# Kernel tuning notes

Measured on AMD Instinct MI355X. Metric: run time of the kernel, lower is better.

## Reference

```python
import jax, jax.numpy as jnp
import numpy as np

B, T, D, H = 4, 1024, 1024, 16
HD = D // H
DFF = 2048          # ExpertTier hidden width
K = 3               # ConvTier causal kernel size
NEG = -1e9


def layernorm(x, w, b, eps=1e-5):
    m = jnp.mean(x, axis=-1, keepdims=True)
    v = jnp.var(x, axis=-1, keepdims=True)
    return (x - m) * jax.lax.rsqrt(v + eps) * w + b


def rope_cos_sin(t, hd):
    inv = 1.0 / (10000.0 ** (jnp.arange(0, hd, 2, dtype=jnp.float32) / hd))
    freqs = jnp.outer(jnp.arange(t, dtype=jnp.float32), inv)  # (T, hd/2)
    return jnp.cos(freqs), jnp.sin(freqs)


def apply_rope(x, cos, sin):
    # x: (B, H, T, hd); cos/sin: (T, hd/2)
    x1, x2 = jnp.split(x, 2, axis=-1)
    return jnp.concatenate([x1 * cos - x2 * sin, x1 * sin + x2 * cos], axis=-1)


def causal_attn(q, k, v):
    # q,k,v: (..., T, d); full causal softmax attention
    t = q.shape[-2]
    scale = 1.0 / jnp.sqrt(jnp.asarray(q.shape[-1], q.dtype))
    scores = jnp.einsum('...qd,...kd->...qk', q, k) * scale
    mask = jnp.triu(jnp.ones((t, t), dtype=bool), k=1)
    scores = jnp.where(mask, NEG, scores)
    w = jax.nn.softmax(scores, axis=-1)
    return jnp.einsum('...qk,...kd->...qd', w, v)


def setup_inputs() -> dict:
    key = jax.random.key(0)
    ks = jax.random.split(key, 16)
    ws = 0.02
    g = lambda k, shape, s: jax.random.normal(k, shape, dtype=jnp.float32) * s
    return {
        'x': g(ks[0], (B, T, D), 1.0),
        'ln1_w': jnp.ones((D,), jnp.float32), 'ln1_b': jnp.zeros((D,), jnp.float32),
        'qkv_w': g(ks[1], (D, 3 * D), ws),
        'out_w': g(ks[2], (D, D), ws),
        'ln2_w': jnp.ones((D,), jnp.float32), 'ln2_b': jnp.zeros((D,), jnp.float32),
        'router_w': g(ks[3], (D, 4), ws),
        'conv_w': g(ks[4], (D, 1, K), 0.1),             # depthwise OIW, groups=D
        'expert_w1': g(ks[5], (D, DFF), ws),
        'expert_w2': g(ks[6], (DFF, D), ws),
        'at_wq': g(ks[7], (D, D), ws),
        'at_wk': g(ks[8], (D, D), ws),
        'at_wv': g(ks[9], (D, D), ws),
        'at_wo': g(ks[10], (D, D), ws),
        'tier_gate': jnp.full((D,), 0.1, jnp.float32),
        'sink_kv_scale': jnp.asarray(0.1, jnp.float32),
    }


def reference(x, ln1_w, ln1_b, qkv_w, out_w, ln2_w, ln2_b, router_w, conv_w,
              expert_w1, expert_w2, at_wq, at_wk, at_wv, at_wo,
              tier_gate, sink_kv_scale):
    b, t, d = x.shape
    # --- backbone causal self-attention with RoPE (pre-norm) ---
    h1 = layernorm(x, ln1_w, ln1_b)
    qkv = (h1 @ qkv_w).reshape(b, t, 3, H, HD)
    q = qkv[:, :, 0].transpose(0, 2, 1, 3)  # (B,H,T,hd)
    k = qkv[:, :, 1].transpose(0, 2, 1, 3)
    v = qkv[:, :, 2].transpose(0, 2, 1, 3)
    cos, sin = rope_cos_sin(t, HD)
    q = apply_rope(q, cos, sin)
    k = apply_rope(k, cos, sin)
    ao = causal_attn(q, k, v)                         # (B,H,T,hd)
    ao = ao.transpose(0, 2, 1, 3).reshape(b, t, d) @ out_w
    x = x + ao
    # --- router + tiers ---
    h = layernorm(x, ln2_w, ln2_b)
    routing_w = jax.nn.softmax(h @ router_w, axis=-1)  # (B,T,4): conv/expert/attn/sink
    # ConvTier: depthwise causal conv (k=3) + GELU
    hc = jnp.pad(h.transpose(0, 2, 1), ((0, 0), (0, 0), (K - 1, 0)))  # (B,D,T+K-1)
    conv = jax.lax.conv_general_dilated(hc, conv_w, (1,), 'VALID',
                                        feature_group_count=d,
                                        dimension_numbers=('NCH', 'OIH', 'NCH'))
    conv_out = jax.nn.gelu(conv.transpose(0, 2, 1))   # (B,T,D)
    # ExpertTier: 2-layer GELU MLP
    expert_out = jax.nn.gelu(h @ expert_w1) @ expert_w2
    # AttentionTier: single-head causal attention
    attn2 = causal_attn(h @ at_wq, h @ at_wk, h @ at_wv) @ at_wo
    # SinkTier outputs zeros -> contributes nothing to the weighted sum
    combined = (conv_out * routing_w[..., 0:1]
                + expert_out * routing_w[..., 1:2]
                + attn2 * routing_w[..., 2:3])
    x = x + combined * tier_gate
    # sink kv scaling
    kv_scale = 1.0 - routing_w[..., 3] * (1.0 - jnp.abs(sink_kv_scale))
    x = x * kv_scale[..., None]
    return (x, routing_w)
```

## Files before the change

kernel.cpp:

```cpp
#include <hip/hip_runtime.h>

#define Bz 4
#define Tz 1024
#define Dz 1024
#define Hz 16
#define NTz (Bz*Tz)

typedef short s8v __attribute__((ext_vector_type(8)));
typedef float f4v __attribute__((ext_vector_type(4)));

__device__ __forceinline__ float bf2f(unsigned short u){
  unsigned int x = ((unsigned int)u) << 16;
  return __builtin_bit_cast(float, x);
}
__device__ __forceinline__ unsigned short f2bf(float f){
  unsigned int x = __builtin_bit_cast(unsigned int, f);
  x += 0x7fffu + ((x >> 16) & 1u);
  return (unsigned short)(x >> 16);
}
__device__ __forceinline__ float gelu_f(float x){
  float z = 1.5957691216057308f * (x + 0.044715f * x * x * x);
  return x / (1.0f + __expf(-z));
}
__device__ __forceinline__ void gl16(const unsigned short* g, unsigned short* l){
  __builtin_amdgcn_global_load_lds(
      (const __attribute__((address_space(1))) unsigned int*)g,
      (__attribute__((address_space(3))) unsigned int*)l, 16, 0, 0);
}

struct WSeg { const float* in; unsigned short* out; int R, C, blk0, bx; };
struct WPack { WSeg s[8]; };
__global__ __launch_bounds__(256) void k_convtrans_all(WPack p)
{
  __shared__ float tile[32][33];
  int bid = blockIdx.x;
  const float* in = p.s[0].in; unsigned short* out = p.s[0].out;
  int R = p.s[0].R, C = p.s[0].C, blk0 = 0, bx = p.s[0].bx;
  #pragma unroll
  for (int i = 1; i < 8; ++i) {
    if (bid >= p.s[i].blk0) {
      in = p.s[i].in; out = p.s[i].out; R = p.s[i].R; C = p.s[i].C;
      blk0 = p.s[i].blk0; bx = p.s[i].bx;
    }
  }
  int rel = bid - blk0;
  int c0 = (rel % bx) * 32, r0 = (rel / bx) * 32;
  int tx = threadIdx.x & 31, ty = threadIdx.x >> 5;
  #pragma unroll
  for (int i = 0; i < 32; i += 8)
    tile[ty + i][tx] = in[(long)(r0 + ty + i) * C + c0 + tx];
  __syncthreads();
  #pragma unroll
  for (int i = 0; i < 32; i += 8)
    out[(long)(c0 + ty + i) * R + r0 + tx] = f2bf(tile[tx][ty + i]);
}

__global__ __launch_bounds__(256) void k_layernorm(const float* __restrict__ x,
    const float* __restrict__ w, const float* __restrict__ b,
    unsigned short* __restrict__ out)
{
  int row = blockIdx.x, tid = threadIdx.x;
  const float4* xp = (const float4*)(x + (long)row * Dz);
  float4 v = xp[tid];
  float s  = v.x + v.y + v.z + v.w;
  float ss = v.x*v.x + v.y*v.y + v.z*v.z + v.w*v.w;
  int lane = tid & 63, wv = tid >> 6;
  #pragma unroll
  for (int off = 32; off; off >>= 1){ s += __shfl_xor(s, off); ss += __shfl_xor(ss, off); }
  __shared__ float red[8];
  if (lane == 0){ red[wv] = s; red[4 + wv] = ss; }
  __syncthreads();
  s  = red[0] + red[1] + red[2] + red[3];
  ss = red[4] + red[5] + red[6] + red[7];
  float mean = s * (1.0f / Dz);
  float var  = ss * (1.0f / Dz) - mean * mean;
  float rstd = rsqrtf(var + 1e-5f);
  float4 wg = ((const float4*)w)[tid];
  float4 bg = ((const float4*)b)[tid];
  ushort4 ov;
  ov.x = f2bf((v.x - mean) * rstd * wg.x + bg.x);
  ov.y = f2bf((v.y - mean) * rstd * wg.y + bg.y);
  ov.z = f2bf((v.z - mean) * rstd * wg.z + bg.z);
  ov.w = f2bf((v.w - mean) * rstd * wg.w + bg.w);
  *((ushort4*)(out + (long)row * Dz) + tid) = ov;
}

__global__ __launch_bounds__(256) void k_ln_router(const unsigned short* __restrict__ x2,
    const float* __restrict__ w, const float* __restrict__ b,
    const float* __restrict__ rw, unsigned short* __restrict__ out,
    float* __restrict__ rout)
{
  int row = blockIdx.x, tid = threadIdx.x;
  ushort4 xu = *((const ushort4*)(x2 + (long)row * Dz) + tid);
  float4 v = {bf2f(xu.x), bf2f(xu.y), bf2f(xu.z), bf2f(xu.w)};
  float s  = v.x + v.y + v.z + v.w;
  float ss = v.x*v.x + v.y*v.y + v.z*v.z + v.w*v.w;
  int lane = tid & 63, wv = tid >> 6;
  #pragma unroll
  for (int off = 32; off; off >>= 1){ s += __shfl_xor(s, off); ss += __shfl_xor(ss, off); }
  __shared__ float red[8];
  if (lane == 0){ red[wv] = s; red[4 + wv] = ss; }
  __syncthreads();
  s  = red[0] + red[1] + red[2] + red[3];
  ss = red[4] + red[5] + red[6] + red[7];
  float mean = s * (1.0f / Dz);
  float var  = ss * (1.0f / Dz) - mean * mean;
  float rstd = rsqrtf(var + 1e-5f);
  float4 wg = ((const float4*)w)[tid];
  float4 bg = ((const float4*)b)[tid];
  float h0 = (v.x - mean) * rstd * wg.x + bg.x;
  float h1 = (v.y - mean) * rstd * wg.y + bg.y;
  float h2 = (v.z - mean) * rstd * wg.z + bg.z;
  float h3 = (v.w - mean) * rstd * wg.w + bg.w;
  ushort4 ov;
  ov.x = f2bf(h0); ov.y = f2bf(h1); ov.z = f2bf(h2); ov.w = f2bf(h3);
  *((ushort4*)(out + (long)row * Dz) + tid) = ov;
  int d0 = tid * 4;
  float4 r0 = *(const float4*)(rw + (long)d0 * 4);
  float4 r1 = *(const float4*)(rw + (long)(d0 + 1) * 4);
  float4 r2 = *(const float4*)(rw + (long)(d0 + 2) * 4);
  float4 r3 = *(const float4*)(rw + (long)(d0 + 3) * 4);
  float a0 = h0*r0.x + h1*r1.x + h2*r2.x + h3*r3.x;
  float a1 = h0*r0.y + h1*r1.y + h2*r2.y + h3*r3.y;
  float a2 = h0*r0.z + h1*r1.z + h2*r2.z + h3*r3.z;
  float a3 = h0*r0.w + h1*r1.w + h2*r2.w + h3*r3.w;
  #pragma unroll
  for (int off = 32; off; off >>= 1) {
    a0 += __shfl_xor(a0, off); a1 += __shfl_xor(a1, off);
    a2 += __shfl_xor(a2, off); a3 += __shfl_xor(a3, off);
  }
  __shared__ float red2[4][4];
  if (lane == 0){ red2[wv][0] = a0; red2[wv][1] = a1; red2[wv][2] = a2; red2[wv][3] = a3; }
  __syncthreads();
  if (tid == 0) {
    float s0 = red2[0][0] + red2[1][0] + red2[2][0] + red2[3][0];
    float s1 = red2[0][1] + red2[1][1] + red2[2][1] + red2[3][1];
    float s2 = red2[0][2] + red2[1][2] + red2[2][2] + red2[3][2];
    float s3 = red2[0][3] + red2[1][3] + red2[2][3] + red2[3][3];
    float mx = fmaxf(fmaxf(s0, s1), fmaxf(s2, s3));
    float e0 = __expf(s0 - mx), e1 = __expf(s1 - mx);
    float e2 = __expf(s2 - mx), e3 = __expf(s3 - mx);
    float inv = 1.0f / (e0 + e1 + e2 + e3);
    float4 r = {e0 * inv, e1 * inv, e2 * inv, e3 * inv};
    *(float4*)(rout + (long)row * 4) = r;
  }
}

__global__ __launch_bounds__(512) void k_gemm512(
    const unsigned short* __restrict__ A,
    const unsigned short* __restrict__ Bt,
    unsigned short* __restrict__ Cb)
{
  constexpr int BK = 64;
  __shared__ unsigned short As[2][128 * BK];
  __shared__ unsigned short Bs[2][128 * BK];
  int lin = blockIdx.y * gridDim.x + blockIdx.x;
  int cols = gridDim.x, rows = gridDim.y;
  int nwg = cols * rows;
  if ((nwg & 7) == 0) lin = (lin & 7) * (nwg >> 3) + (lin >> 3);
  int in_grp = 8 * cols;
  int gid = lin / in_grp;
  int fm = gid * 8;
  int gsz = min(rows - fm, 8);
  int rem = lin - gid * in_grp;
  int pm = fm + (rem % gsz);
  int pn = rem / gsz;
  int bm = pm * 128, bn = pn * 128;

  int tid = threadIdx.x, w = tid >> 6, lane = tid & 63;
  int fr = lane & 15, fg = lane >> 4;
  int sw = (fr & 7) * 8;
  int wr = (w >> 1) * 32, wc = (w & 1) * 64;
  int lrow = lane >> 3;
  int lcol = ((lane & 7) ^ lrow) * 8;

  const unsigned short* AgJ[2];
  const unsigned short* BgJ[2];
  int OffJ[2];
  #pragma unroll
  for (int j = 0; j < 2; ++j) {
    AgJ[j] = A  + (long)(bm + j * 64 + w * 8 + lrow) * 1024 + lcol;
    BgJ[j] = Bt + (long)(bn + j * 64 + w * 8 + lrow) * 1024 + lcol;
    OffJ[j] = (j * 64 + w * 8) * BK;
  }

  f4v acc[2][4];
  #pragma unroll
  for (int m = 0; m < 2; ++m)
    #pragma unroll
    for (int n = 0; n < 4; ++n)
      acc[m][n] = (f4v){0.f, 0.f, 0.f, 0.f};

  auto stage = [&](int buf, int k0){
    #pragma unroll
    for (int j = 0; j < 2; ++j) gl16(AgJ[j] + k0, &As[buf][OffJ[j]]);
    #pragma unroll
    for (int j = 0; j < 2; ++j) gl16(BgJ[j] + k0, &Bs[buf][OffJ[j]]);
  };
  auto compute = [&](int buf){
    #pragma unroll
    for (int kk = 0; kk < 2; ++kk) {
      int kg = (kk * 32 + fg * 8) ^ sw;
      s8v af[2], bfv[4];
      #pragma unroll
      for (int m = 0; m < 2; ++m) af[m]  = *(const s8v*)&As[buf][(wr + m * 16 + fr) * BK + kg];
      #pragma unroll
      for (int n = 0; n < 4; ++n) bfv[n] = *(const s8v*)&Bs[buf][(wc + n * 16 + fr) * BK + kg];
      #pragma unroll
      for (int m = 0; m < 2; ++m)
        #pragma unroll
        for (int n = 0; n < 4; ++n)
          acc[m][n] = __builtin_amdgcn_mfma_f32_16x16x32_bf16(af[m], bfv[n], acc[m][n], 0, 0, 0);
    }
  };

  int cur = 0;
  stage(0, 0);
  __syncthreads();
  for (int k0 = 0; k0 < 1024; k0 += BK) {
    if (k0 + BK < 1024) stage(cur ^ 1, k0 + BK);
    compute(cur);
    __syncthreads();
    cur ^= 1;
  }

  int cr = bm + wr + fg * 4, cc = bn + wc + fr;
  #pragma unroll
  for (int m = 0; m < 2; ++m)
    #pragma unroll
    for (int n = 0; n < 4; ++n)
      #pragma unroll
      for (int i = 0; i < 4; ++i) {
        long row = cr + m * 16 + i;
        long col = cc + n * 16;
        float v = acc[m][n][i];
        if (col < 2048) v = gelu_f(v);
        Cb[row * 5120 + col] = f2bf(v);
      }
}

__global__ __launch_bounds__(512) void k_tail512(
    const unsigned short* __restrict__ tierb,
    const unsigned short* __restrict__ w_ew2t,
    unsigned short* __restrict__ eo, long eoDelta,
    unsigned short* __restrict__ Sb,
    unsigned short* __restrict__ v2t)
{
  constexpr int BK = 64;
  __shared__ unsigned short As[2][128 * BK];
  __shared__ unsigned short Bs[2][128 * BK];
  int bid = blockIdx.x;
  int tid = threadIdx.x;

  if (bid >= 656) {
    int g0 = (bid - 656) * 16;
    int sub = tid & 255, half = tid >> 8;
    int tx = sub & 31, ty = sub >> 5;
    unsigned short* T = &As[0][0] + half * 1100;
    for (int it = 0; it < 8; ++it) {
      int g = g0 + half * 8 + it;
      int z = g >> 10, rem = g & 1023;
      int r0 = (rem >> 5) * 32, c0 = (rem & 31) * 32;
      const unsigned short* inp = tierb + 4096 + (long)z * ((long)Tz * 5120);
      unsigned short* outp = v2t + (long)z * ((long)Tz * 1024);
      #pragma unroll
      for (int i = 0; i < 32; i += 8)
        T[(ty + i) * 33 + tx] = inp[(long)(r0 + ty + i) * 5120 + c0 + tx];
      __syncthreads();
      #pragma unroll
      for (int i = 0; i < 32; i += 8)
        outp[(long)(c0 + ty + i) * 1024 + r0 + tx] = T[tx * 33 + (ty + i)];
      __syncthreads();
    }
    return;
  }

  int w = tid >> 6, lane = tid & 63;
  int fr = lane & 15, fg = lane >> 4;
  int sw = (fr & 7) * 8;
  int wr = (w >> 1) * 32, wc = (w & 1) * 64;
  int lrow = lane >> 3;
  int lcol = ((lane & 7) ^ lrow) * 8;

  const unsigned short* A;
  const unsigned short* Bt;
  unsigned short* Cout;
  long ldA, ldB;
  int bm, bn;
  float scale;
  if (bid < 512) {
    int z = bid >> 8;
    int lin = bid & 255;
    lin = (lin & 7) * 32 + (lin >> 3);
    int gid = lin / 64;
    int fm = gid * 8;
    int rem = lin - gid * 64;
    int pm = fm + (rem & 7);
    int pn = rem >> 3;
    bm = pm * 128; bn = pn * 128;
    A    = tierb + (long)z * 1024;
    Bt   = w_ew2t + (long)z * 1024;
    Cout = eo + (long)z * eoDelta;
    ldA = 5120; ldB = 2048;
    scale = 1.0f;
  } else {
    int r2 = bid - 512;
    int li = r2 % 36;
    int z  = r2 / 36;
    int r = (int)((sqrtf(8.f * li + 1.f) - 1.f) * 0.5f);
    if ((r + 1) * (r + 2) / 2 <= li) ++r;
    if (r * (r + 1) / 2 > li) --r;
    bm = r * 128; bn = (li - r * (r + 1) / 2) * 128;
    A    = tierb + 2048 + (long)z * ((long)Tz * 5120);
    Bt   = tierb + 3072 + (long)z * ((long)Tz * 5120);
    Cout = Sb + (long)z * ((long)Tz * Tz);
    ldA = 5120; ldB = 5120;
    scale = 0.03125f;
  }

  const unsigned short* AgJ[2];
  const unsigned short* BgJ[2];
  int OffJ[2];
  #pragma unroll
  for (int j = 0; j < 2; ++j) {
    AgJ[j] = A  + (long)(bm + j * 64 + w * 8 + lrow) * ldA + lcol;
    BgJ[j] = Bt + (long)(bn + j * 64 + w * 8 + lrow) * ldB + lcol;
    OffJ[j] = (j * 64 + w * 8) * BK;
  }

  f4v acc[2][4];
  #pragma unroll
  for (int m = 0; m < 2; ++m)
    #pragma unroll
    for (int n = 0; n < 4; ++n)
      acc[m][n] = (f4v){0.f, 0.f, 0.f, 0.f};

  auto stage = [&](int buf, int k0){
    #pragma unroll
    for (int j = 0; j < 2; ++j) gl16(AgJ[j] + k0, &As[buf][OffJ[j]]);
    #pragma unroll
    for (int j = 0; j < 2; ++j) gl16(BgJ[j] + k0, &Bs[buf][OffJ[j]]);
  };
  auto compute = [&](int buf){
    #pragma unroll
    for (int kk = 0; kk < 2; ++kk) {
      int kg = (kk * 32 + fg * 8) ^ sw;
      s8v af[2], bfv[4];
      #pragma unroll
      for (int m = 0; m < 2; ++m) af[m]  = *(const s8v*)&As[buf][(wr + m * 16 + fr) * BK + kg];
      #pragma unroll
      for (int n = 0; n < 4; ++n) bfv[n] = *(const s8v*)&Bs[buf][(wc + n * 16 + fr) * BK + kg];
      #pragma unroll
      for (int m = 0; m < 2; ++m)
        #pragma unroll
        for (int n = 0; n < 4; ++n)
          acc[m][n] = __builtin_amdgcn_mfma_f32_16x16x32_bf16(af[m], bfv[n], acc[m][n], 0, 0, 0);
    }
  };

  int cur = 0;
  stage(0, 0);
  __syncthreads();
  for (int k0 = 0; k0 < 1024; k0 += BK) {
    if (k0 + BK < 1024) stage(cur ^ 1, k0 + BK);
    compute(cur);
    __syncthreads();
    cur ^= 1;
  }

  int cr = bm + wr + fg * 4, cc = bn + wc + fr;
  #pragma unroll
  for (int m = 0; m < 2; ++m)
    #pragma unroll
    for (int n = 0; n < 4; ++n)
      #pragma unroll
      for (int i = 0; i < 4; ++i) {
        long row = cr + m * 16 + i;
        long col = cc + n * 16;
        Cout[row * 1024 + col] = f2bf(acc[m][n][i] * scale);
      }
}

__global__ __launch_bounds__(512) void k_wo512(
    const unsigned short* __restrict__ A,
    const unsigned short* __restrict__ Bt,
    unsigned short* __restrict__ Cb, long sC)
{
  constexpr int BK = 64;
  __shared__ unsigned short As[2][128 * BK];
  __shared__ unsigned short Bs[2][128 * BK];
  A  += (long)blockIdx.z * 512;
  Bt += (long)blockIdx.z * 512;
  Cb += (long)blockIdx.z * sC;
  int lin = blockIdx.y * gridDim.x + blockIdx.x;
  int cols = gridDim.x, rows = gridDim.y;
  int nwg = cols * rows;
  if ((nwg & 7) == 0) lin = (lin & 7) * (nwg >> 3) + (lin >> 3);
  int in_grp = 8 * cols;
  int gid = lin / in_grp;
  int fm = gid * 8;
  int gsz = min(rows - fm, 8);
  int rem = lin - gid * in_grp;
  int pm = fm + (rem % gsz);
  int pn = rem / gsz;
  int bm = pm * 128, bn = pn * 128;

  int tid = threadIdx.x, w = tid >> 6, lane = tid & 63;
  int fr = lane & 15, fg = lane >> 4;
  int sw = (fr & 7) * 8;
  int wr = (w >> 1) * 32, wc = (w & 1) * 64;
  int lrow = lane >> 3;
  int lcol = ((lane & 7) ^ lrow) * 8;

  const unsigned short* AgJ[2];
  const unsigned short* BgJ[2];
  int OffJ[2];
  #pragma unroll
  for (int j = 0; j < 2; ++j) {
    AgJ[j] = A  + (long)(bm + j * 64 + w * 8 + lrow) * 1024 + lcol;
    BgJ[j] = Bt + (long)(bn + j * 64 + w * 8 + lrow) * 1024 + lcol;
    OffJ[j] = (j * 64 + w * 8) * BK;
  }

  f4v acc[2][4];
  #pragma unroll
  for (int m = 0; m < 2; ++m)
    #pragma unroll
    for (int n = 0; n < 4; ++n)
      acc[m][n] = (f4v){0.f, 0.f, 0.f, 0.f};

  auto stage = [&](int buf, int k0){
    #pragma unroll
    for (int j = 0; j < 2; ++j) gl16(AgJ[j] + k0, &As[buf][OffJ[j]]);
    #pragma unroll
    for (int j = 0; j < 2; ++j) gl16(BgJ[j] + k0, &Bs[buf][OffJ[j]]);
  };
  auto compute = [&](int buf){
    #pragma unroll
    for (int kk = 0; kk < 2; ++kk) {
      int kg = (kk * 32 + fg * 8) ^ sw;
      s8v af[2], bfv[4];
      #pragma unroll
      for (int m = 0; m < 2; ++m) af[m]  = *(const s8v*)&As[buf][(wr + m * 16 + fr) * BK + kg];
      #pragma unroll
      for (int n = 0; n < 4; ++n) bfv[n] = *(const s8v*)&Bs[buf][(wc + n * 16 + fr) * BK + kg];
      #pragma unroll
      for (int m = 0; m < 2; ++m)
        #pragma unroll
        for (int n = 0; n < 4; ++n)
          acc[m][n] = __builtin_amdgcn_mfma_f32_16x16x32_bf16(af[m], bfv[n], acc[m][n], 0, 0, 0);
    }
  };

  int cur = 0;
  stage(0, 0);
  __syncthreads();
  for (int k0 = 0; k0 < 512; k0 += BK) {
    if (k0 + BK < 512) stage(cur ^ 1, k0 + BK);
    compute(cur);
    __syncthreads();
    cur ^= 1;
  }

  int cr = bm + wr + fg * 4, cc = bn + wc + fr;
  #pragma unroll
  for (int m = 0; m < 2; ++m)
    #pragma unroll
    for (int n = 0; n < 4; ++n)
      #pragma unroll
      for (int i = 0; i < 4; ++i) {
        long row = cr + m * 16 + i;
        long col = cc + n * 16;
        Cb[row * 1024 + col] = f2bf(acc[m][n][i]);
      }
}

template<int MODE, int BN, bool TRIMAP, bool TRIK, bool DBUF>
__global__ __launch_bounds__(256) void k_gemm(
    const unsigned short* __restrict__ A,
    const unsigned short* __restrict__ Bt,
    float* __restrict__ Cf, unsigned short* __restrict__ Cb,
    const float* __restrict__ addsrc,
    unsigned short* __restrict__ P1, unsigned short* __restrict__ P2,
    int N, int K, int lda, int ldb,
    long sA, long sB, long sC)
{
  constexpr int BM = 128;
  constexpr int MREP = (BN == 128) ? 4 : 2;
  constexpr int NB = DBUF ? 2 : 1;
  __shared__ unsigned short As[NB][BM * 64];
  __shared__ unsigned short Bs[NB][BN * 64];
  int bm, bn;
  if (TRIMAP) {
    int li = blockIdx.x;
    int nwg = gridDim.x;
    if ((nwg & 7) == 0) li = (li & 7) * (nwg >> 3) + (li >> 3);
    int r = (int)((sqrtf(4.f * li + 1.f) - 1.f) * 0.5f);
    if ((r + 1) * (r + 2) <= li) ++r;
    if (r * (r + 1) > li) --r;
    bm = r * 128; bn = (li - r * (r + 1)) * BN;
  } else {
    int lin = blockIdx.y * gridDim.x + blockIdx.x;
    int nwg = gridDim.x * gridDim.y;
    if ((nwg & 7) == 0) lin = (lin & 7) * (nwg >> 3) + (lin >> 3);
    int cols = gridDim.x, rows = gridDim.y;
    constexpr int GM = 8;
    int in_grp = GM * cols;
    int gid = lin / in_grp;
    int fm = gid * GM;
    int gsz = min(rows - fm, GM);
    int rem = lin - gid * in_grp;
    int pm = fm + (rem % gsz);
    int pn = rem / gsz;
    if (TRIK) pm = rows - 1 - pm;
    bm = pm * BM; bn = pn * BN;
  }
  A  += (long)blockIdx.z * sA;
  Bt += (long)blockIdx.z * sB;
  int tid = threadIdx.x, w = tid >> 6, lane = tid & 63;
  int wr, wc;
  if (BN == 128) { wr = (w >> 1) * 64; wc = (w & 1) * 64; }
  else           { wr = w * 32;        wc = 0; }
  f4v acc[MREP][4];
  #pragma unroll
  for (int m = 0; m < MREP; ++m)
    #pragma unroll
    for (int n = 0; n < 4; ++n)
      acc[m][n] = (f4v){0.f, 0.f, 0.f, 0.f};

  int Keff = K;
  if (TRIK) Keff = min(K, bm + BM);

  int lrow = lane >> 3;
  int lcol = (((lane & 7) ^ lrow) * 8);
  const unsigned short* AgJ[4];
  int AsOff[4];
  #pragma unroll
  for (int j = 0; j < 4; ++j) {
    AgJ[j] = A + (long)(bm + w * 32 + j * 8 + lrow) * lda + lcol;
    AsOff[j] = (w * 32 + j * 8) * 64;
  }
  constexpr int BCH = BN / 8 / 4;
  const unsigned short* BgJ[BCH];
  int BsOff[BCH];
  #pragma unroll
  for (int j = 0; j < BCH; ++j) {
    BgJ[j] = Bt + (long)(bn + w * (BCH * 8) + j * 8 + lrow) * ldb + lcol;
    BsOff[j] = (w * (BCH * 8) + j * 8) * 64;
  }

  int fr = lane & 15, fg = lane >> 4;
  int sw = (fr & 7) * 8;

  auto stage = [&](int buf, int k0){
    #pragma unroll
    for (int j = 0; j < 4; ++j) gl16(AgJ[j] + k0, &As[buf][AsOff[j]]);
    #pragma unroll
    for (int j = 0; j < BCH; ++j) gl16(BgJ[j] + k0, &Bs[buf][BsOff[j]]);
  };
  auto compute = [&](int buf){
    #pragma unroll
    for (int kk = 0; kk < 2; ++kk) {
      int kg = (kk * 32 + fg * 8) ^ sw;
      s8v af[MREP], bfv[4];
      #pragma unroll
      for (int m = 0; m < MREP; ++m) af[m]  = *(const s8v*)&As[buf][(wr + m * 16 + fr) * 64 + kg];
      #pragma unroll
      for (int n = 0; n < 4; ++n)    bfv[n] = *(const s8v*)&Bs[buf][(wc + n * 16 + fr) * 64 + kg];
      #pragma unroll
      for (int m = 0; m < MREP; ++m)
        #pragma unroll
        for (int n = 0; n < 4; ++n)
          acc[m][n] = __builtin_amdgcn_mfma_f32_16x16x32_bf16(af[m], bfv[n], acc[m][n], 0, 0, 0);
    }
  };

  if (DBUF) {
    int cur = 0;
    stage(0, 0);
    __syncthreads();
    for (int k0 = 0; k0 < Keff; k0 += 64) {
      if (k0 + 64 < Keff) stage(cur ^ 1, k0 + 64);
      compute(cur);
      __syncthreads();
      cur ^= 1;
    }
  } else {
    for (int k0 = 0; k0 < Keff; k0 += 64) {
      __syncthreads();
      stage(0, k0);
      __syncthreads();
      compute(0);
    }
  }

  int cr0 = bm + wr + fg * 4;
  int cc0 = bn + wc + fr;

  if (MODE == 4) {
    int sect = bn >> 10;
    if (sect == 2) {
      #pragma unroll
      for (int m = 0; m < MREP; ++m)
        #pragma unroll
        for (int n = 0; n < 4; ++n)
          #pragma unroll
          for (int i = 0; i < 4; ++i) {
            int row = cr0 + m * 16 + i;
            int vcol = (bn - 2048) + wc + n * 16 + fr;
            P2[(long)row * 1024 + vcol] = f2bf(acc[m][n][i]);
          }
    } else {
      unsigned short* dst = (sect == 0) ? Cb : P1;
      float scl = (sect == 0) ? 0.125f : 1.0f;
      int head = ((bn & 1023) + wc) >> 6;
      float inv0 = exp2f(-(float)fr * 0.4152410118609203f);
      float inv1 = exp2f(-(float)(fr + 16) * 0.4152410118609203f);
      #pragma unroll
      for (int m = 0; m < MREP; ++m)
        #pragma unroll
        for (int i = 0; i < 4; ++i) {
          int row = cr0 + m * 16 + i;
          int t = row & 1023, bq = row >> 10;
          float a0 = (float)t * inv0, a1 = (float)t * inv1;
          float cs0 = __cosf(a0), sn0 = __sinf(a0);
          float cs1 = __cosf(a1), sn1 = __sinf(a1);
          float v0 = acc[m][0][i], v1 = acc[m][1][i];
          float v2 = acc[m][2][i], v3 = acc[m][3][i];
          long base = ((long)(bq * 16 + head)) * 65536 + (long)t * 64 + fr;
          dst[base]      = f2bf((v0 * cs0 - v2 * sn0) * scl);
          dst[base + 32] = f2bf((v0 * sn0 + v2 * cs0) * scl);
          dst[base + 16] = f2bf((v1 * cs1 - v3 * sn1) * scl);
          dst[base + 48] = f2bf((v1 * sn1 + v3 * cs1) * scl);
        }
    }
    return;
  }

  #pragma unroll
  for (int m = 0; m < MREP; ++m)
    #pragma unroll
    for (int n = 0; n < 4; ++n)
      #pragma unroll
      for (int i = 0; i < 4; ++i) {
        long row = cr0 + m * 16 + i, col = cc0 + n * 16;
        long idx = (long)blockIdx.z * sC + row * (long)N + col;
        float v = acc[m][n][i];
        if (MODE == 1 || MODE == 7) v += addsrc[idx];
        if (MODE == 6) v *= 0.03125f;
        if (MODE <= 1) Cf[idx] = v; else Cb[idx] = f2bf(v);
      }
}

__global__ __launch_bounds__(256) void k_attn_mfma(
    const unsigned short* __restrict__ Qb, const unsigned short* __restrict__ Kb,
    const unsigned short* __restrict__ Vt, unsigned short* __restrict__ ao)
{
  __shared__ unsigned short Ks[64][72];
  __shared__ unsigned short Vs[64][72];
  __shared__ unsigned short Ps[4][16][72];
  int qb = 15 - (blockIdx.x >> 6);
  int bh = blockIdx.x & 63;
  int b = bh >> 4, h = bh & 15;
  int t0 = qb * 64;
  int tid = threadIdx.x, w = tid >> 6, lane = tid & 63;
  int fr = lane & 15, fg = lane >> 4;

  const unsigned short* qp = Qb + (long)bh * Tz * 64 + (long)(t0 + w * 16 + fr) * 64 + fg * 8;
  s8v qf[2] = { *(const s8v*)qp, *(const s8v*)(qp + 32) };

  f4v o_acc[4];
  #pragma unroll
  for (int n = 0; n < 4; ++n) o_acc[n] = (f4v){0.f, 0.f, 0.f, 0.f};
  float m_[4] = {-1e30f, -1e30f, -1e30f, -1e30f};
  float l_[4] = {0.f, 0.f, 0.f, 0.f};

  int sr = tid >> 3, sc = (tid & 7) * 8;
  const unsigned short* Kg = Kb + (long)bh * Tz * 64 + (long)sr * 64 + sc;
  const unsigned short* Vg = Vt + (long)bh * 64 * Tz + (long)sr * Tz + sc;

  uint4 pk0, pk1, pv0, pv1;
  auto loadregs = [&](int k0){
    pk0 = *(const uint4*)(Kg + (long)k0 * 64);
    pk1 = *(const uint4*)(Kg + (long)(k0 + 32) * 64);
    pv0 = *(const uint4*)(Vg + k0);
    pv1 = *(const uint4*)(Vg + (long)32 * Tz + k0);
  };
  auto storelds = [&](){
    *(uint4*)&Ks[sr][sc]      = pk0;
    *(uint4*)&Ks[sr + 32][sc] = pk1;
    *(uint4*)&Vs[sr][sc]      = pv0;
    *(uint4*)&Vs[sr + 32][sc] = pv1;
  };

  loadregs(0);
  storelds();
  __syncthreads();

  for (int kt = 0; kt <= qb; ++kt) {
    int k0 = kt * 64;
    if (kt < qb) loadregs(k0 + 64);

    f4v sacc[4];
    #pragma unroll
    for (int n = 0; n < 4; ++n) sacc[n] = (f4v){0.f, 0.f, 0.f, 0.f};
    #pragma unroll
    for (int kk = 0; kk < 2; ++kk) {
      int kg = kk * 32 + fg * 8;
      #pragma unroll
      for (int n = 0; n < 4; ++n) {
        s8v bf = *(const s8v*)&Ks[n * 16 + fr][kg];
        sacc[n] = __builtin_amdgcn_mfma_f32_16x16x32_bf16(qf[kk], bf, sacc[n], 0, 0, 0);
      }
    }

    bool full = (kt < qb);
    float p[4][4], alpha[4];
    #pragma unroll
    for (int i = 0; i < 4; ++i) {
      int trow = t0 + w * 16 + fg * 4 + i;
      float mx = -1e30f;
      #pragma unroll
      for (int n = 0; n < 4; ++n) {
        float sval = sacc[n][i];
        if (!full) {
          int key = k0 + n * 16 + fr;
          sval = (key <= trow) ? sval : -1e30f;
        }
        p[n][i] = sval;
        mx = fmaxf(mx, sval);
      }
      mx = fmaxf(mx, __shfl_xor(mx, 1));
      mx = fmaxf(mx, __shfl_xor(mx, 2));
      mx = fmaxf(mx, __shfl_xor(mx, 4));
      mx = fmaxf(mx, __shfl_xor(mx, 8));
      float mnew = fmaxf(m_[i], mx);
      alpha[i] = __expf(m_[i] - mnew);
      m_[i] = mnew;
      float ps = 0.f;
      #pragma unroll
      for (int n = 0; n < 4; ++n) {
        float pv = __expf(p[n][i] - mnew);
        p[n][i] = pv;
        ps += pv;
      }
      ps += __shfl_xor(ps, 1); ps += __shfl_xor(ps, 2);
      ps += __shfl_xor(ps, 4); ps += __shfl_xor(ps, 8);
      l_[i] = l_[i] * alpha[i] + ps;
    }
    #pragma unroll
    for (int n = 0; n < 4; ++n)
      #pragma unroll
      for (int i = 0; i < 4; ++i)
        o_acc[n][i] *= alpha[i];
    #pragma unroll
    for (int n = 0; n < 4; ++n)
      #pragma unroll
      for (int i = 0; i < 4; ++i)
        Ps[w][fg * 4 + i][n * 16 + fr] = f2bf(p[n][i]);

    #pragma unroll
    for (int kk = 0; kk < 2; ++kk) {
      int kg = kk * 32 + fg * 8;
      s8v pa = *(const s8v*)&Ps[w][fr][kg];
      #pragma unroll
      for (int n = 0; n < 4; ++n) {
        s8v vb = *(const s8v*)&Vs[n * 16 + fr][kg];
        o_acc[n] = __builtin_amdgcn_mfma_f32_16x16x32_bf16(pa, vb, o_acc[n], 0, 0, 0);
      }
    }

    if (kt < qb) {
      __syncthreads();
      storelds();
      __syncthreads();
    }
  }

  float inv[4];
  #pragma unroll
  for (int i = 0; i < 4; ++i) inv[i] = 1.0f / l_[i];
  #pragma unroll
  for (int n = 0; n < 4; ++n)
    #pragma unroll
    for (int i = 0; i < 4; ++i) {
      int t = t0 + w * 16 + fg * 4 + i;
      ao[((long)(b * Tz + t)) * Dz + h * 64 + n * 16 + fr] = f2bf(o_acc[n][i] * inv[i]);
    }
}

__global__ __launch_bounds__(256) void k_softmax_causal(const unsigned short* __restrict__ S,
    unsigned short* __restrict__ P)
{
  long row = blockIdx.x;
  int t = (int)(row & (Tz - 1));
  int tid = threadIdx.x;
  const unsigned short* sp = S + row * Tz;
  ushort4 v = ((const ushort4*)sp)[tid];
  float vv[4];
  vv[0] = (tid*4 + 0 <= t) ? bf2f(v.x) : -1e30f;
  vv[1] = (tid*4 + 1 <= t) ? bf2f(v.y) : -1e30f;
  vv[2] = (tid*4 + 2 <= t) ? bf2f(v.z) : -1e30f;
  vv[3] = (tid*4 + 3 <= t) ? bf2f(v.w) : -1e30f;
  float mx = fmaxf(fmaxf(vv[0], vv[1]), fmaxf(vv[2], vv[3]));
  int lane = tid & 63, wv = tid >> 6;
  #pragma unroll
  for (int off = 32; off; off >>= 1) mx = fmaxf(mx, __shfl_xor(mx, off));
  __shared__ float red[8];
  if (lane == 0) red[wv] = mx;
  __syncthreads();
  mx = fmaxf(fmaxf(red[0], red[1]), fmaxf(red[2], red[3]));
  float p[4];
  float s = 0.f;
  #pragma unroll
  for (int i = 0; i < 4; ++i){ p[i] = __expf(vv[i] - mx); s += p[i]; }
  #pragma unroll
  for (int off = 32; off; off >>= 1) s += __shfl_xor(s, off);
  if (lane == 0) red[4 + wv] = s;
  __syncthreads();
  s = red[4] + red[5] + red[6] + red[7];
  float inv = 1.0f / s;
  ushort4 ov;
  ov.x = f2bf(p[0] * inv); ov.y = f2bf(p[1] * inv);
  ov.z = f2bf(p[2] * inv); ov.w = f2bf(p[3] * inv);
  *((ushort4*)(P + row * Tz) + tid) = ov;
}

__global__ __launch_bounds__(256) void k_combine(
    const unsigned short* __restrict__ x2, const unsigned short* __restrict__ hbf,
    const unsigned short* __restrict__ eoa, const unsigned short* __restrict__ eob,
    const unsigned short* __restrict__ ap, const unsigned short* __restrict__ ap2,
    const float* __restrict__ rout, const float* __restrict__ convw,
    const float* __restrict__ tg, const float* __restrict__ sinkp,
    float* __restrict__ outx)
{
  int row = blockIdx.x, tid = threadIdx.x;
  int t = row & (Tz - 1), b = row >> 10;
  int d0 = tid * 4;
  ushort4 xu = *(const ushort4*)(x2 + (long)row * Dz + d0);
  ushort4 ea = *(const ushort4*)(eoa + (long)row * Dz + d0);
  ushort4 eb = *(const ushort4*)(eob + (long)row * Dz + d0);
  ushort4 a4 = *(const ushort4*)(ap + (long)row * Dz + d0);
  ushort4 a42 = *(const ushort4*)(ap2 + (long)row * Dz + d0);
  float4 t4 = *(const float4*)(tg + d0);
  float4 r4 = *(const float4*)(rout + (long)row * 4);
  float sks = fabsf(sinkp[0]);
  float kv = 1.0f - r4.w * (1.0f - sks);
  const float4* cwp = (const float4*)(convw + (long)d0 * 3);
  float4 c0 = cwp[0], c1 = cwp[1], c2 = cwp[2];
  float cwf[12] = {c0.x, c0.y, c0.z, c0.w, c1.x, c1.y, c1.z, c1.w, c2.x, c2.y, c2.z, c2.w};
  float hv[3][4];
  #pragma unroll
  for (int tap = 0; tap < 3; ++tap) {
    int tt = t - 2 + tap;
    if (tt >= 0) {
      ushort4 hu = *((const ushort4*)(hbf + ((long)(b * Tz + tt)) * Dz + d0));
      hv[tap][0] = bf2f(hu.x); hv[tap][1] = bf2f(hu.y);
      hv[tap][2] = bf2f(hu.z); hv[tap][3] = bf2f(hu.w);
    } else {
      hv[tap][0] = 0.f; hv[tap][1] = 0.f; hv[tap][2] = 0.f; hv[tap][3] = 0.f;
    }
  }
  float ov[4];
  float xi[4] = {bf2f(xu.x), bf2f(xu.y), bf2f(xu.z), bf2f(xu.w)};
  float ei[4] = {bf2f(ea.x) + bf2f(eb.x), bf2f(ea.y) + bf2f(eb.y),
                 bf2f(ea.z) + bf2f(eb.z), bf2f(ea.w) + bf2f(eb.w)};
  float ai[4] = {bf2f(a4.x) + bf2f(a42.x), bf2f(a4.y) + bf2f(a42.y),
                 bf2f(a4.z) + bf2f(a42.z), bf2f(a4.w) + bf2f(a42.w)};
  float ti[4] = {t4.x, t4.y, t4.z, t4.w};
  #pragma unroll
  for (int i = 0; i < 4; ++i) {
    float conv = hv[0][i] * cwf[i*3 + 0] + hv[1][i] * cwf[i*3 + 1] + hv[2][i] * cwf[i*3 + 2];
    float comb = gelu_f(conv) * r4.x + ei[i] * r4.y + ai[i] * r4.z;
    ov[i] = (xi[i] + comb * ti[i]) * kv;
  }
  float4 res = {ov[0], ov[1], ov[2], ov[3]};
  *(float4*)(outx + (long)row * Dz + d0) = res;
}

extern "C" void kernel_launch(void* const* d_in, const int* in_sizes, int n_in,
                              void* d_out, int out_size, void* d_ws, size_t ws_size,
                              hipStream_t stream) {
  (void)in_sizes; (void)n_in; (void)out_size; (void)ws_size;
  const float* x       = (const float*)d_in[0];
  const float* ln1_w   = (const float*)d_in[1];
  const float* ln1_b   = (const float*)d_in[2];
  const float* qkv_w   = (const float*)d_in[3];
  const float* out_w   = (const float*)d_in[4];
  const float* ln2_w   = (const float*)d_in[5];
  const float* ln2_b   = (const float*)d_in[6];
  const float* router_w= (const float*)d_in[7];
  const float* conv_w  = (const float*)d_in[8];
  const float* ew1     = (const float*)d_in[9];
  const float* ew2     = (const float*)d_in[10];
  const float* at_wq   = (const float*)d_in[11];
  const float* at_wk   = (const float*)d_in[12];
  const float* at_wv   = (const float*)d_in[13];
  const float* at_wo   = (const float*)d_in[14];
  const float* tg      = (const float*)d_in[15];
  const float* sinkp   = (const float*)d_in[16];
  float* outx = (float*)d_out;
  float* rout = outx + (size_t)NTz * Dz;

  char* ws = (char*)d_ws;
  size_t off = 0;
  auto alloc = [&](size_t bytes) -> char* {
    char* p = ws + off;
    off += (bytes + 255) & ~(size_t)255;
    return p;
  };
  const long TD = (long)Tz * Dz, TT = (long)Tz * Tz;

  unsigned short* w_qkvt  = (unsigned short*)alloc((size_t)3072*1024*2);
  unsigned short* w_outt  = (unsigned short*)alloc((size_t)1024*1024*2);
  unsigned short* w_tiert = (unsigned short*)alloc((size_t)5120*1024*2);
  unsigned short* w_ew2t  = (unsigned short*)alloc((size_t)1024*2048*2);
  unsigned short* w_wot   = (unsigned short*)alloc((size_t)1024*1024*2);
  unsigned short* h1bf    = (unsigned short*)alloc((size_t)NTz*Dz*2);
  unsigned short* tierb   = (unsigned short*)alloc((size_t)NTz*5120*2);
  unsigned short* aobf    = (unsigned short*)alloc((size_t)NTz*Dz*2);
  unsigned short* x2b     = (unsigned short*)alloc((size_t)NTz*Dz*2);
  unsigned short* hbf     = (unsigned short*)alloc((size_t)NTz*Dz*2);
  unsigned short* Pbf     = (unsigned short*)alloc((size_t)Bz*Tz*Tz*2);
  unsigned short* v2tbf   = (unsigned short*)alloc((size_t)NTz*Dz*2);
  unsigned short* a2obf   = (unsigned short*)alloc((size_t)NTz*Dz*2);
  unsigned short* eofb    = (unsigned short*)alloc((size_t)NTz*Dz*2);
  unsigned short* a2pb    = (unsigned short*)alloc((size_t)NTz*Dz*2);
  unsigned short* Sbf     = (unsigned short*)alloc((size_t)Bz*Tz*Tz*2);

  unsigned short* Qb = x2b;
  unsigned short* Kb = Pbf;
  unsigned short* Vb = tierb;
  unsigned short* Vt = a2pb;
  unsigned short* eofb2 = h1bf;
  long eoDelta = (long)(eofb2 - eofb);
  unsigned short* a2pb2 = Sbf;
  long woDelta = (long)(a2pb2 - a2pb);

  dim3 blk(256);

  WPack wp;
  wp.s[0] = {qkv_w, w_qkvt,                         1024, 3072, 0,     96};
  wp.s[1] = {out_w, w_outt,                         1024, 1024, 3072,  32};
  wp.s[2] = {ew1,   w_tiert,                        1024, 2048, 4096,  64};
  wp.s[3] = {at_wq, w_tiert + 2048*1024,            1024, 1024, 6144,  32};
  wp.s[4] = {at_wk, w_tiert + 3072*1024,            1024, 1024, 7168,  32};
  wp.s[5] = {at_wv, w_tiert + (size_t)4096*1024,    1024, 1024, 8192,  32};
  wp.s[6] = {ew2,   w_ew2t,                         2048, 1024, 9216,  32};
  wp.s[7] = {at_wo, w_wot,                          1024, 1024, 11264, 32};
  k_convtrans_all<<<dim3(12288), blk, 0, stream>>>(wp);

  k_layernorm<<<NTz, blk, 0, stream>>>(x, ln1_w, ln1_b, h1bf);
  k_gemm<4,128,false,false,true><<<dim3(24, 32), blk, 0, stream>>>(h1bf, w_qkvt,
      nullptr, Qb, nullptr, Kb, Vb, 3072, 1024, 1024, 1024, 0, 0, 0);
  {
  }
  extern __global__ void k_vt_bb(const unsigned short*, unsigned short*);
  k_vt_bb<<<dim3(4096), blk, 0, stream>>>(Vb, Vt);
  k_attn_mfma<<<dim3(1024), blk, 0, stream>>>(Qb, Kb, Vt, aobf);
  k_gemm<7,64,false,false,true><<<dim3(16, 32), blk, 0, stream>>>(aobf, w_outt, nullptr,
      x2b, x, nullptr, nullptr, 1024, 1024, 1024, 1024, 0, 0, 0);
  k_ln_router<<<NTz, blk, 0, stream>>>(x2b, ln2_w, ln2_b, router_w, hbf, rout);
  k_gemm512<<<dim3(40, 32), dim3(512), 0, stream>>>(hbf, w_tiert, tierb);
  k_tail512<<<dim3(912), dim3(512), 0, stream>>>(tierb, w_ew2t, eofb, eoDelta,
      Sbf, v2tbf);
  k_softmax_causal<<<NTz, blk, 0, stream>>>(Sbf, Pbf);
  k_gemm<3,64,false,true,true><<<dim3(16, 8, 4), blk, 0, stream>>>(Pbf, v2tbf, nullptr,
      a2obf, nullptr, nullptr, nullptr, 1024, 1024, 1024, 1024, TT, TD, TD);
  k_wo512<<<dim3(8, 32, 2), dim3(512), 0, stream>>>(a2obf, w_wot, a2pb, woDelta);
  k_combine<<<NTz, blk, 0, stream>>>(x2b, hbf, eofb, eofb2, a2pb, a2pb2, rout,
      conv_w, tg, sinkp, outx);
}

__global__ __launch_bounds__(256) void k_vt_bb(const unsigned short* __restrict__ in,
    unsigned short* __restrict__ out)
{
  __shared__ unsigned short tile[32][34];
  int bidc = blockIdx.x & 31;
  int bidr = blockIdx.x >> 5;
  int c0 = bidc * 32, r0 = bidr * 32;
  int tx = threadIdx.x & 31, ty = threadIdx.x >> 5;
  #pragma unroll
  for (int i = 0; i < 32; i += 8)
    tile[ty + i][tx] = in[(long)(r0 + ty + i) * 1024 + c0 + tx];
  __syncthreads();
  #pragma unroll
  for (int i = 0; i < 32; i += 8) {
    int c = c0 + ty + i;
    int r = r0 + tx;
    int b = r >> 10, t = r & 1023;
    int bh = b * 16 + (c >> 6), d = c & 63;
    out[((long)bh * 64 + d) * Tz + t] = tile[tx][ty + i];
  }
}
```

Baseline: 267.3 us.

## Split QKV GEMM into plain 512-thread GEMM plus fused RoPE/transpose kernel

Replaces the generic QKV GEMM, whose MODE 4 epilogue applied RoPE with scattered stores, and the separate V-transpose kernel. The new path is a dedicated 512-thread bf16 MFMA GEMM with a grouped tile order that writes a plain row-major QKV buffer. A second kernel then applies RoPE to Q and K with vectorized loads and stores and transposes V through LDS. The goal is coalesced epilogue stores, better L2 reuse, and one fewer dedicated transpose pass. In exchange, Q, K and V now take an extra full round trip through memory.

```diff
diff --git a/kernel.cpp b/kernel.cpp
--- a/kernel.cpp
+++ b/kernel.cpp
@@ -237,6 +237,147 @@
         if (col < 2048) v = gelu_f(v);
         Cb[row * 5120 + col] = f2bf(v);
       }
+}
+
+__global__ __launch_bounds__(512) void k_qkv512(
+    const unsigned short* __restrict__ A,
+    const unsigned short* __restrict__ Bt,
+    unsigned short* __restrict__ Cb)
+{
+  constexpr int BK = 64;
+  __shared__ unsigned short As[2][128 * BK];
+  __shared__ unsigned short Bs[2][128 * BK];
+  int lin = blockIdx.y * gridDim.x + blockIdx.x;
+  int cols = gridDim.x, rows = gridDim.y;
+  int nwg = cols * rows;
+  if ((nwg & 7) == 0) lin = (lin & 7) * (nwg >> 3) + (lin >> 3);
+  int in_grp = 8 * cols;
+  int gid = lin / in_grp;
+  int fm = gid * 8;
+  int gsz = min(rows - fm, 8);
+  int rem = lin - gid * in_grp;
+  int pm = fm + (rem % gsz);
+  int pn = rem / gsz;
+  int bm = pm * 128, bn = pn * 128;
+
+  int tid = threadIdx.x, w = tid >> 6, lane = tid & 63;
+  int fr = lane & 15, fg = lane >> 4;
+  int sw = (fr & 7) * 8;
+  int wr = (w >> 1) * 32, wc = (w & 1) * 64;
+  int lrow = lane >> 3;
+  int lcol = ((lane & 7) ^ lrow) * 8;
+
+  const unsigned short* AgJ[2];
+  const unsigned short* BgJ[2];
+  int OffJ[2];
+  #pragma unroll
+  for (int j = 0; j < 2; ++j) {
+    AgJ[j] = A  + (long)(bm + j * 64 + w * 8 + lrow) * 1024 + lcol;
+    BgJ[j] = Bt + (long)(bn + j * 64 + w * 8 + lrow) * 1024 + lcol;
+    OffJ[j] = (j * 64 + w * 8) * BK;
+  }
+
+  f4v acc[2][4];
+  #pragma unroll
+  for (int m = 0; m < 2; ++m)
+    #pragma unroll
+    for (int n = 0; n < 4; ++n)
+      acc[m][n] = (f4v){0.f, 0.f, 0.f, 0.f};
+
+  auto stage = [&](int buf, int k0){
+    #pragma unroll
+    for (int j = 0; j < 2; ++j) gl16(AgJ[j] + k0, &As[buf][OffJ[j]]);
+    #pragma unroll
+    for (int j = 0; j < 2; ++j) gl16(BgJ[j] + k0, &Bs[buf][OffJ[j]]);
+  };
+  auto compute = [&](int buf){
+    #pragma unroll
+    for (int kk = 0; kk < 2; ++kk) {
+      int kg = (kk * 32 + fg * 8) ^ sw;
+      s8v af[2], bfv[4];
+      #pragma unroll
+      for (int m = 0; m < 2; ++m) af[m]  = *(const s8v*)&As[buf][(wr + m * 16 + fr) * BK + kg];
+      #pragma unroll
+      for (int n = 0; n < 4; ++n) bfv[n] = *(const s8v*)&Bs[buf][(wc + n * 16 + fr) * BK + kg];
+      #pragma unroll
+      for (int m = 0; m < 2; ++m)
+        #pragma unroll
+        for (int n = 0; n < 4; ++n)
+          acc[m][n] = __builtin_amdgcn_mfma_f32_16x16x32_bf16(af[m], bfv[n], acc[m][n], 0, 0, 0);
+    }
+  };
+
+  int cur = 0;
+  stage(0, 0);
+  __syncthreads();
+  for (int k0 = 0; k0 < 1024; k0 += BK) {
+    if (k0 + BK < 1024) stage(cur ^ 1, k0 + BK);
+    compute(cur);
+    __syncthreads();
+    cur ^= 1;
+  }
+
+  int cr = bm + wr + fg * 4, cc = bn + wc + fr;
+  #pragma unroll
+  for (int m = 0; m < 2; ++m)
+    #pragma unroll
+    for (int n = 0; n < 4; ++n)
+      #pragma unroll
+      for (int i = 0; i < 4; ++i) {
+        long row = cr + m * 16 + i;
+        long col = cc + n * 16;
+        Cb[row * 3072 + col] = f2bf(acc[m][n][i]);
+      }
+}
+
+__global__ __launch_bounds__(256) void k_qkvsplit(const unsigned short* __restrict__ qkv,
+    unsigned short* __restrict__ Qb, unsigned short* __restrict__ Kb,
+    unsigned short* __restrict__ Vt)
+{
+  __shared__ unsigned short vt_s[64][40];
+  int t0 = blockIdx.x * 32;
+  int bh = blockIdx.y;
+  int b = bh >> 4, h = bh & 15;
+  int tid = threadIdx.x;
+  int tl = tid >> 3, jb = (tid & 7) * 4;
+  int t = t0 + tl;
+  long base = ((long)(b * Tz + t)) * 3072 + h * 64;
+  float cs[4], sn[4];
+  #pragma unroll
+  for (int ii = 0; ii < 4; ++ii) {
+    float inv = exp2f(-(float)(jb + ii) * 0.41524101186092030f);
+    sincosf((float)t * inv, &sn[ii], &cs[ii]);
+  }
+  ushort4 q1 = *(const ushort4*)(qkv + base + jb);
+  ushort4 q2 = *(const ushort4*)(qkv + base + jb + 32);
+  ushort4 k1 = *(const ushort4*)(qkv + base + 1024 + jb);
+  ushort4 k2 = *(const ushort4*)(qkv + base + 1024 + jb + 32);
+  ushort4 v1 = *(const ushort4*)(qkv + base + 2048 + jb);
+  ushort4 v2 = *(const ushort4*)(qkv + base + 2048 + jb + 32);
+  float q1a[4] = {bf2f(q1.x), bf2f(q1.y), bf2f(q1.z), bf2f(q1.w)};
+  float q2a[4] = {bf2f(q2.x), bf2f(q2.y), bf2f(q2.z), bf2f(q2.w)};
+  float k1a[4] = {bf2f(k1.x), bf2f(k1.y), bf2f(k1.z), bf2f(k1.w)};
+  float k2a[4] = {bf2f(k2.x), bf2f(k2.y), bf2f(k2.z), bf2f(k2.w)};
+  unsigned short va[4] = {v1.x, v1.y, v1.z, v1.w};
+  unsigned short vb[4] = {v2.x, v2.y, v2.z, v2.w};
+  unsigned short qo1[4], qo2[4], ko1[4], ko2[4];
+  #pragma unroll
+  for (int ii = 0; ii < 4; ++ii) {
+    qo1[ii] = f2bf((q1a[ii] * cs[ii] - q2a[ii] * sn[ii]) * 0.125f);
+    qo2[ii] = f2bf((q1a[ii] * sn[ii] + q2a[ii] * cs[ii]) * 0.125f);
+    ko1[ii] = f2bf(k1a[ii] * cs[ii] - k2a[ii] * sn[ii]);
+    ko2[ii] = f2bf(k1a[ii] * sn[ii] + k2a[ii] * cs[ii]);
+    vt_s[jb + ii][tl]      = va[ii];
+    vt_s[jb + 32 + ii][tl] = vb[ii];
+  }
+  long ob = (long)bh * Tz * 64 + (long)t * 64;
+  *(ushort4*)(Qb + ob + jb)      = *(ushort4*)qo1;
+  *(ushort4*)(Qb + ob + jb + 32) = *(ushort4*)qo2;
+  *(ushort4*)(Kb + ob + jb)      = *(ushort4*)ko1;
+  *(ushort4*)(Kb + ob + jb + 32) = *(ushort4*)ko2;
+  __syncthreads();
+  int d = tid >> 2, tc = (tid & 3) * 8;
+  *(uint4*)(Vt + (long)bh * 64 * Tz + (long)d * Tz + t0 + tc) = *(const uint4*)&vt_s[d][tc];
 }
 
 __global__ __launch_bounds__(512) void k_tail512(
@@ -597,46 +738,6 @@
   int cr0 = bm + wr + fg * 4;
   int cc0 = bn + wc + fr;
 
-  if (MODE == 4) {
-    int sect = bn >> 10;
-    if (sect == 2) {
-      #pragma unroll
-      for (int m = 0; m < MREP; ++m)
-        #pragma unroll
-        for (int n = 0; n < 4; ++n)
-          #pragma unroll
-          for (int i = 0; i < 4; ++i) {
-            int row = cr0 + m * 16 + i;
-            int vcol = (bn - 2048) + wc + n * 16 + fr;
-            P2[(long)row * 1024 + vcol] = f2bf(acc[m][n][i]);
-          }
-    } else {
-      unsigned short* dst = (sect == 0) ? Cb : P1;
-      float scl = (sect == 0) ? 0.125f : 1.0f;
-      int head = ((bn & 1023) + wc) >> 6;
-      float inv0 = exp2f(-(float)fr * 0.4152410118609203f);
-      float inv1 = exp2f(-(float)(fr + 16) * 0.4152410118609203f);
-      #pragma unroll
-      for (int m = 0; m < MREP; ++m)
-        #pragma unroll
-        for (int i = 0; i < 4; ++i) {
-          int row = cr0 + m * 16 + i;
-          int t = row & 1023, bq = row >> 10;
-          float a0 = (float)t * inv0, a1 = (float)t * inv1;
-          float cs0 = __cosf(a0), sn0 = __sinf(a0);
-          float cs1 = __cosf(a1), sn1 = __sinf(a1);
-          float v0 = acc[m][0][i], v1 = acc[m][1][i];
-          float v2 = acc[m][2][i], v3 = acc[m][3][i];
-          long base = ((long)(bq * 16 + head)) * 65536 + (long)t * 64 + fr;
-          dst[base]      = f2bf((v0 * cs0 - v2 * sn0) * scl);
-          dst[base + 32] = f2bf((v0 * sn0 + v2 * cs0) * scl);
-          dst[base + 16] = f2bf((v1 * cs1 - v3 * sn1) * scl);
-          dst[base + 48] = f2bf((v1 * sn1 + v3 * cs1) * scl);
-        }
-    }
-    return;
-  }
-
   #pragma unroll
   for (int m = 0; m < MREP; ++m)
     #pragma unroll
@@ -928,9 +1029,9 @@
   unsigned short* a2pb    = (unsigned short*)alloc((size_t)NTz*Dz*2);
   unsigned short* Sbf     = (unsigned short*)alloc((size_t)Bz*Tz*Tz*2);
 
+  unsigned short* qkvb = tierb;
   unsigned short* Qb = x2b;
   unsigned short* Kb = Pbf;
-  unsigned short* Vb = tierb;
   unsigned short* Vt = a2pb;
   unsigned short* eofb2 = h1bf;
   long eoDelta = (long)(eofb2 - eofb);
@@ -951,12 +1052,8 @@
   k_convtrans_all<<<dim3(12288), blk, 0, stream>>>(wp);
 
   k_layernorm<<<NTz, blk, 0, stream>>>(x, ln1_w, ln1_b, h1bf);
-  k_gemm<4,128,false,false,true><<<dim3(24, 32), blk, 0, stream>>>(h1bf, w_qkvt,
-      nullptr, Qb, nullptr, Kb, Vb, 3072, 1024, 1024, 1024, 0, 0, 0);
-  {
-  }
-  extern __global__ void k_vt_bb(const unsigned short*, unsigned short*);
-  k_vt_bb<<<dim3(4096), blk, 0, stream>>>(Vb, Vt);
+  k_qkv512<<<dim3(24, 32), dim3(512), 0, stream>>>(h1bf, w_qkvt, qkvb);
+  k_qkvsplit<<<dim3(32, 64), blk, 0, stream>>>(qkvb, Qb, Kb, Vt);
   k_attn_mfma<<<dim3(1024), blk, 0, stream>>>(Qb, Kb, Vt, aobf);
   k_gemm<7,64,false,false,true><<<dim3(16, 32), blk, 0, stream>>>(aobf, w_outt, nullptr,
       x2b, x, nullptr, nullptr, 1024, 1024, 1024, 1024, 0, 0, 0);
@@ -971,25 +1068,3 @@
   k_combine<<<NTz, blk, 0, stream>>>(x2b, hbf, eofb, eofb2, a2pb, a2pb2, rout,
       conv_w, tg, sinkp, outx);
 }
-
-__global__ __launch_bounds__(256) void k_vt_bb(const unsigned short* __restrict__ in,
-    unsigned short* __restrict__ out)
-{
-  __shared__ unsigned short tile[32][34];
-  int bidc = blockIdx.x & 31;
-  int bidr = blockIdx.x >> 5;
-  int c0 = bidc * 32, r0 = bidr * 32;
-  int tx = threadIdx.x & 31, ty = threadIdx.x >> 5;
-  #pragma unroll
-  for (int i = 0; i < 32; i += 8)
-    tile[ty + i][tx] = in[(long)(r0 + ty + i) * 1024 + c0 + tx];
-  __syncthreads();
-  #pragma unroll
-  for (int i = 0; i < 32; i += 8) {
-    int c = c0 + ty + i;
-    int r = r0 + tx;
-    int b = r >> 10, t = r & 1023;
-    int bh = b * 16 + (c >> 6), d = c & 63;
-    out[((long)bh * 64 + d) * Tz + t] = tile[tx][ty + i];
-  }
-}
```

Result: faster. 262.1 us (-2.0%).
